# Optimization experiments

Measured on AMD Instinct MI355X. Metric: run time of the kernel, lower is better.

## Reference

```python
import jax, jax.numpy as jnp
import numpy as np

FM = 256          # feature_maps
ROUNDS = 32
N_VARS = 4000
N_CLAUSES = 16800 # ~4.2 * n_vars (3-SAT phase transition)
K = 3             # literals per clause
EPS = 1e-8


def setup_inputs() -> dict:
    key = jax.random.key(0)
    ks = jax.random.split(key, 20)

    def nrm(k, shape):
        # tf.initializers.RandomNormal default stddev = 0.05
        return jax.random.normal(k, shape, jnp.float32) * 0.05

    vs = jax.random.randint(ks[0], (N_CLAUSES, K), 1, N_VARS + 1)
    sg = jnp.where(jax.random.uniform(ks[1], (N_CLAUSES, K)) < 0.5, -1, 1)
    return {
        "clause_lits": (vs * sg).astype(jnp.int32),  # signed 1-based literals
        "n_vars": N_VARS,
        "L_init": nrm(ks[2], (1, FM)), "C_init": nrm(ks[3], (1, FM)),
        "LC_W0": nrm(ks[4], (FM, FM)), "LC_b0": jnp.zeros((FM,), jnp.float32),
        "LC_W1": nrm(ks[5], (FM, FM)), "LC_b1": jnp.zeros((FM,), jnp.float32),
        "LC_W2": nrm(ks[6], (FM, FM)), "LC_b2": jnp.zeros((FM,), jnp.float32),
        "CL_W0": nrm(ks[7], (FM, FM)), "CL_b0": jnp.zeros((FM,), jnp.float32),
        "CL_W1": nrm(ks[8], (FM, FM)), "CL_b1": jnp.zeros((FM,), jnp.float32),
        "CL_W2": nrm(ks[9], (FM, FM)), "CL_b2": jnp.zeros((FM,), jnp.float32),
        "C_Wx": nrm(ks[10], (FM, 4 * FM)), "C_Wh": nrm(ks[11], (FM, 4 * FM)),
        "C_b": jnp.zeros((4 * FM,), jnp.float32),
        "L_Wx": nrm(ks[12], (2 * FM, 4 * FM)), "L_Wh": nrm(ks[13], (FM, 4 * FM)),
        "L_b": jnp.zeros((4 * FM,), jnp.float32),
        "V_W0": nrm(ks[14], (2 * FM, 2 * FM)), "V_b0": jnp.zeros((2 * FM,), jnp.float32),
        "V_W1": nrm(ks[15], (2 * FM, 2 * FM)), "V_b1": jnp.zeros((2 * FM,), jnp.float32),
        "V_W2": nrm(ks[16], (2 * FM, 1)), "V_b2": jnp.zeros((1,), jnp.float32),
    }


def _mlp3(x, W0, b0, W1, b1, W2, b2):
    h = jax.nn.relu(x @ W0 + b0)
    h = jax.nn.relu(h @ W1 + b1)
    return h @ W2 + b2


def _lstm(x, h, c, Wx, Wh, b):
    # keras LSTMCell: gate order i, f, g, o; sigmoid recurrent, tanh activation
    z = x @ Wx + h @ Wh + b
    i, f, g, o = jnp.split(z, 4, axis=1)
    c = jax.nn.sigmoid(f) * c + jax.nn.sigmoid(i) * jnp.tanh(g)
    h = jax.nn.sigmoid(o) * jnp.tanh(c)
    return h, c


def reference(clause_lits, n_vars, L_init, C_init,
              LC_W0, LC_b0, LC_W1, LC_b1, LC_W2, LC_b2,
              CL_W0, CL_b0, CL_W1, CL_b1, CL_W2, CL_b2,
              C_Wx, C_Wh, C_b, L_Wx, L_Wh, L_b,
              V_W0, V_b0, V_W1, V_b1, V_W2, V_b2):
    n_clauses = clause_lits.shape[0]
    n_lits = 2 * n_vars
    lits = clause_lits.reshape(-1)                         # [E]
    sign = jnp.sign(lits).astype(jnp.float32)              # [E]
    var_idx = jnp.abs(lits) - 1                            # [E] 0-based var
    lit_idx = jnp.where(lits > 0, var_idx, n_vars + var_idx)
    clause_idx = jnp.repeat(jnp.arange(n_clauses), clause_lits.shape[1])

    denom = jnp.sqrt(jnp.float32(FM))
    l_h = jnp.tile(L_init / denom, (n_lits, 1))
    c_h = jnp.tile(C_init / denom, (n_clauses, 1))
    l_c = jnp.zeros_like(l_h)
    c_c = jnp.zeros_like(c_h)

    def vote(lh):
        variables = jnp.concatenate([lh[:n_vars], lh[n_vars:]], axis=1)  # [n_vars, 2*FM]
        return _mlp3(variables, V_W0, V_b0, V_W1, V_b1, V_W2, V_b2)      # [n_vars, 1]

    def clause_loss(logits):
        # softplus_log_square_loss: clause_val = exp(-sum_lit softplus(sign*logit))
        vals = logits[var_idx, 0] * sign                   # [E]
        s = jax.ops.segment_sum(jax.nn.softplus(vals), clause_idx,
                                num_segments=n_clauses, indices_are_sorted=True)
        cv = jnp.exp(-s)
        return jnp.sum(jnp.square(-jnp.log(1.0 - cv + EPS)))

    def round_fn(carry, _):
        lh, lc, ch, cc, loss = carry
        lc_pre = _mlp3(lh, LC_W0, LC_b0, LC_W1, LC_b1, LC_W2, LC_b2)
        # SpMM adj^T @ msgs: scatter literal messages into clauses
        lc_msgs = jax.ops.segment_sum(lc_pre[lit_idx], clause_idx,
                                      num_segments=n_clauses, indices_are_sorted=True)
        ch, cc = _lstm(lc_msgs, ch, cc, C_Wx, C_Wh, C_b)
        cl_pre = _mlp3(ch, CL_W0, CL_b0, CL_W1, CL_b1, CL_W2, CL_b2)
        # SpMM adj @ msgs: scatter clause messages into literals
        cl_msgs = jax.ops.segment_sum(cl_pre[clause_idx], lit_idx, num_segments=n_lits)
        flipped = jnp.concatenate([lh[n_vars:], lh[:n_vars]], axis=0)
        lh, lc = _lstm(jnp.concatenate([cl_msgs, flipped], axis=1), lh, lc,
                       L_Wx, L_Wh, L_b)
        loss = loss + clause_loss(vote(lh))
        return (lh, lc, ch, cc, loss), None

    (l_h, l_c, c_h, c_c, loss), _ = jax.lax.scan(
        round_fn, (l_h, l_c, c_h, c_c, jnp.float32(0.0)), None, length=ROUNDS)
    logits = vote(l_h)
    return logits, loss / jnp.float32(ROUNDS)
```

## Files before the change

### kernel.cpp

```cpp
#include <hip/hip_runtime.h>
#include <hip/hip_bf16.h>

#define NV 4000
#define NL 8000
#define NC 16800
#define NE 50400
#define FM 256
#define ROUNDS 32

typedef short s16x8 __attribute__((ext_vector_type(8)));
typedef __bf16 b16x8 __attribute__((ext_vector_type(8)));
typedef float f32x4 __attribute__((ext_vector_type(4)));
union V8 { s16x8 s; b16x8 b; ushort u[8]; };

using gaddr_t = const void __attribute__((address_space(1)))*;
using laddr_t = void __attribute__((address_space(3)))*;

__device__ __forceinline__ float b2f(ushort u) {
    union { uint i; float f; } v; v.i = ((uint)u) << 16; return v.f;
}
__device__ __forceinline__ ushort f2b(float f) {
    __hip_bfloat16 h = __float2bfloat16(f);
    return *(ushort*)&h;
}

__global__ void zero_kernel(float* __restrict__ p, int n) {
    int i = blockIdx.x * blockDim.x + threadIdx.x;
    if (i < n) p[i] = 0.0f;
}
__global__ void f2b_kernel(const float* __restrict__ src, ushort* __restrict__ dst, int n) {
    int i = blockIdx.x * blockDim.x + threadIdx.x;
    if (i < n) dst[i] = f2b(src[i]);
}
__global__ void transpose_w6_kernel(
    const float* __restrict__ s0, const float* __restrict__ s1, const float* __restrict__ s2,
    const float* __restrict__ s3, const float* __restrict__ s4, const float* __restrict__ s5,
    ushort* __restrict__ d0, ushort* __restrict__ d1, ushort* __restrict__ d2,
    ushort* __restrict__ d3, ushort* __restrict__ d4, ushort* __restrict__ d5)
{
    const float* srcs[6] = {s0, s1, s2, s3, s4, s5};
    ushort* dsts[6] = {d0, d1, d2, d3, d4, d5};
    const float* in = srcs[blockIdx.y];
    ushort* out = dsts[blockIdx.y];
    int idx = blockIdx.x * blockDim.x + threadIdx.x;
    int n = idx >> 8, k = idx & 255;
    out[n * 256 + k] = f2b(in[k * 256 + n]);
}
__global__ void transpose_w_kernel(const float* __restrict__ in, ushort* __restrict__ out,
                                   int K, int N, int ldo, int koff, int perm) {
    int idx = blockIdx.x * blockDim.x + threadIdx.x;
    if (idx >= K * N) return;
    int n = idx / K, k = idx - n * K;
    int row = perm ? ((n & 255) * 4 + (n >> 8)) : n;
    out[(size_t)row * ldo + koff + k] = f2b(in[(size_t)k * N + n]);
}
__global__ void permute_bias_kernel(const float* __restrict__ b, float* __restrict__ bp) {
    int n = blockIdx.x * blockDim.x + threadIdx.x;
    if (n < 1024) bp[(n & 255) * 4 + (n >> 8)] = b[n];
}

__global__ void init_all_kernel(const float* __restrict__ Li, const float* __restrict__ Ci,
                                ushort* __restrict__ lh, float* __restrict__ lc32,
                                ushort* __restrict__ ch, float* __restrict__ cc32) {
    int idx = blockIdx.x * blockDim.x + threadIdx.x;
    if (idx < NL * FM) { lh[idx] = f2b(Li[idx & 255] * (1.0f / 16.0f)); lc32[idx] = 0.0f; }
    if (idx < NC * FM) { ch[idx] = f2b(Ci[idx & 255] * (1.0f / 16.0f)); cc32[idx] = 0.0f; }
}
__global__ void fill_hist_kernel(float* __restrict__ hist, const float* __restrict__ b2,
                                 float* __restrict__ loss_arr) {
    int i = blockIdx.x * blockDim.x + threadIdx.x;
    if (i < ROUNDS * NV) hist[i] = b2[0];
    if (i < ROUNDS) loss_arr[i] = 0.0f;
}

__global__ void csr_count_kernel(const int* __restrict__ lits, int* __restrict__ deg) {
    int e = blockIdx.x * blockDim.x + threadIdx.x;
    if (e >= NE) return;
    int l = lits[e];
    int v = (l > 0 ? l : -l) - 1;
    int li = (l > 0) ? v : NV + v;
    atomicAdd(&deg[li], 1);
}
__global__ __launch_bounds__(1024) void csr_scan_kernel(const int* __restrict__ deg,
                                                        int* __restrict__ rowptr,
                                                        int* __restrict__ nxt) {
    __shared__ int ls[1024];
    int t = threadIdx.x;
    int base = t * 8;
    int local[8];
    int s = 0;
    #pragma unroll
    for (int i = 0; i < 8; ++i) {
        int idx = base + i;
        int d = (idx < NL) ? deg[idx] : 0;
        local[i] = s;
        s += d;
    }
    ls[t] = s;
    __syncthreads();
    for (int st = 1; st < 1024; st <<= 1) {
        int v = (t >= st) ? ls[t - st] : 0;
        __syncthreads();
        ls[t] += v;
        __syncthreads();
    }
    int prefix = (t == 0) ? 0 : ls[t - 1];
    #pragma unroll
    for (int i = 0; i < 8; ++i) {
        int idx = base + i;
        if (idx < NL) { int v = prefix + local[i]; rowptr[idx] = v; nxt[idx] = v; }
    }
    if (t == 1023) rowptr[NL] = ls[1023];
}
__global__ void csr_fill_kernel(const int* __restrict__ lits, int* __restrict__ nxt,
                                int* __restrict__ ecl) {
    int e = blockIdx.x * blockDim.x + threadIdx.x;
    if (e >= NE) return;
    int l = lits[e];
    int v = (l > 0 ? l : -l) - 1;
    int li = (l > 0) ? v : NV + v;
    int pos = atomicAdd(&nxt[li], 1);
    ecl[pos] = e / 3;
}

#define BKT 64

#define MLPR 32
__global__ __launch_bounds__(256) void mlp3_kernel(
    const ushort* __restrict__ A,
    const ushort* __restrict__ W0t, const float* __restrict__ b0,
    const ushort* __restrict__ W1t, const float* __restrict__ b1,
    const ushort* __restrict__ W2t, const float* __restrict__ b2,
    ushort* __restrict__ out, int M)
{
    __shared__ __align__(16) ushort As[MLPR * BKT];
    __shared__ __align__(16) ushort Wl[256 * BKT];
    __shared__ __align__(16) ushort Ab[MLPR * 264];
    const int tid = threadIdx.x;
    const int lane = tid & 63, wid = tid >> 6;
    const int rowBase = blockIdx.x * MLPR;
    const int lr = lane >> 3, ql = (lane & 7) ^ lr;
    const int cl16 = lane & 15, kg = lane >> 4;

    const ushort* Wt[3] = {W0t, W1t, W2t};
    const float*  bs[3] = {b0, b1, b2};

    #pragma unroll
    for (int layer = 0; layer < 3; ++layer) {
        f32x4 acc[2][4];
        #pragma unroll
        for (int i = 0; i < 2; ++i)
            #pragma unroll
            for (int j = 0; j < 4; ++j) acc[i][j] = (f32x4){0.f, 0.f, 0.f, 0.f};

        for (int kt = 0; kt < 4; ++kt) {
            __syncthreads();
            #pragma unroll
            for (int t = 0; t < 8; ++t) {
                int row = wid * 64 + t * 8 + lr;
                __builtin_amdgcn_global_load_lds(
                    (gaddr_t)(Wt[layer] + (size_t)row * 256 + kt * 64 + ql * 8),
                    (laddr_t)&Wl[(wid * 64 + t * 8) * BKT + lane * 8], 16, 0, 0);
            }
            if (layer == 0) {
                int row = rowBase + wid * 8 + lr;
                if (row > M - 1) row = M - 1;
                __builtin_amdgcn_global_load_lds(
                    (gaddr_t)(A + (size_t)row * 256 + kt * 64 + ql * 8),
                    (laddr_t)&As[wid * 512 + lane * 8], 16, 0, 0);
            }
            __syncthreads();
            #pragma unroll
            for (int s = 0; s < 2; ++s) {
                int kq8 = s * 4 + kg;
                V8 af[2], bf[4];
                #pragma unroll
                for (int i = 0; i < 2; ++i) {
                    int m = i * 16 + cl16;
                    if (layer == 0)
                        af[i].s = *(const s16x8*)&As[m * BKT + ((kq8 ^ (m & 7)) * 8)];
                    else
                        af[i].s = *(const s16x8*)&Ab[m * 264 + kt * 64 + kq8 * 8];
                }
                #pragma unroll
                for (int j = 0; j < 4; ++j) {
                    int n = wid * 64 + j * 16 + cl16;
                    bf[j].s = *(const s16x8*)&Wl[n * BKT + ((kq8 ^ (n & 7)) * 8)];
                }
                #pragma unroll
                for (int i = 0; i < 2; ++i)
                    #pragma unroll
                    for (int j = 0; j < 4; ++j)
                        acc[i][j] = __builtin_amdgcn_mfma_f32_16x16x32_bf16(
                            af[i].b, bf[j].b, acc[i][j], 0, 0, 0);
            }
        }
        __syncthreads();
        const int rq = (lane >> 4) * 4;
        #pragma unroll
        for (int i = 0; i < 2; ++i)
            #pragma unroll
            for (int r = 0; r < 4; ++r) {
                int row = i * 16 + rq + r;
                #pragma unroll
                for (int j = 0; j < 4; ++j) {
                    int col = wid * 64 + j * 16 + cl16;
                    float v = acc[i][j][r] + bs[layer][col];
                    if (layer < 2) {
                        Ab[row * 264 + col] = f2b(fmaxf(v, 0.0f));
                    } else {
                        int grow = rowBase + row;
                        if (grow < M) out[(size_t)grow * 256 + col] = f2b(v);
                    }
                }
            }
    }
}

__global__ __launch_bounds__(256) void gemm16_n64_kernel(
    const ushort* __restrict__ A0, int K0,
    const ushort* __restrict__ A1, int K1,
    const ushort* __restrict__ Bt, const float* __restrict__ bias,
    ushort* __restrict__ C, int M, int N, int relu)
{
    __shared__ __align__(16) ushort Al[128 * BKT];
    __shared__ __align__(16) ushort Bl[64 * BKT];
    const int Ktot = K0 + K1;
    const int tid = threadIdx.x;
    const int rowBase = blockIdx.y * 128, colBase = blockIdx.x * 64;
    const int lane = tid & 63, wid = tid >> 6;
    const int wm = (wid & 1) * 64, wn = (wid >> 1) * 32;
    const int lr = lane >> 3, ql = (lane & 7) ^ lr;

    f32x4 acc[4][2];
    #pragma unroll
    for (int i = 0; i < 4; ++i)
        #pragma unroll
        for (int j = 0; j < 2; ++j) acc[i][j] = (f32x4){0.f, 0.f, 0.f, 0.f};

    for (int k0 = 0; k0 < Ktot; k0 += BKT) {
        const ushort* As; int ks, lda;
        if (k0 < K0) { As = A0; ks = k0; lda = K0; }
        else         { As = A1; ks = k0 - K0; lda = K1; }
        __syncthreads();
        #pragma unroll
        for (int t = 0; t < 4; ++t) {
            int rloc = (wid * 4 + t) * 8 + lr;
            int ga = rowBase + rloc; if (ga > M - 1) ga = M - 1;
            __builtin_amdgcn_global_load_lds((gaddr_t)(As + (size_t)ga * lda + ks + ql * 8),
                                             (laddr_t)&Al[(wid * 4 + t) * 512], 16, 0, 0);
        }
        #pragma unroll
        for (int t = 0; t < 2; ++t) {
            int rloc = (wid * 2 + t) * 8 + lr;
            __builtin_amdgcn_global_load_lds((gaddr_t)(Bt + (size_t)(colBase + rloc) * Ktot + k0 + ql * 8),
                                             (laddr_t)&Bl[(wid * 2 + t) * 512], 16, 0, 0);
        }
        __syncthreads();
        const int cl = lane & 15, kg = lane >> 4;
        #pragma unroll
        for (int s = 0; s < 2; ++s) {
            V8 af[4], bf[2];
            #pragma unroll
            for (int i = 0; i < 4; ++i) {
                int m = wm + i * 16 + cl;
                af[i].s = *(const s16x8*)&Al[m * BKT + (((s * 4 + kg) ^ (m & 7)) * 8)];
            }
            #pragma unroll
            for (int j = 0; j < 2; ++j) {
                int n = wn + j * 16 + cl;
                bf[j].s = *(const s16x8*)&Bl[n * BKT + (((s * 4 + kg) ^ (n & 7)) * 8)];
            }
            #pragma unroll
            for (int i = 0; i < 4; ++i)
                #pragma unroll
                for (int j = 0; j < 2; ++j)
                    acc[i][j] = __builtin_amdgcn_mfma_f32_16x16x32_bf16(af[i].b, bf[j].b,
                                                                        acc[i][j], 0, 0, 0);
        }
    }
    const int rq = (lane >> 4) * 4, cl = lane & 15;
    #pragma unroll
    for (int i = 0; i < 4; ++i)
        #pragma unroll
        for (int r = 0; r < 4; ++r) {
            int grow = rowBase + wm + i * 16 + rq + r;
            if (grow >= M) continue;
            #pragma unroll
            for (int j = 0; j < 2; ++j) {
                int gcol = colBase + wn + j * 16 + cl;
                float v = acc[i][j][r] + bias[gcol];
                if (relu) v = fmaxf(v, 0.0f);
                C[(size_t)grow * N + gcol] = f2b(v);
            }
        }
}

__global__ __launch_bounds__(256) void gemm16_vote_kernel(
    const ushort* __restrict__ A0,
    const ushort* __restrict__ Bt,
    const float* __restrict__ bias,
    const ushort* __restrict__ w2,
    float* __restrict__ logits, int M)
{
    __shared__ __align__(16) ushort Al[128 * BKT];
    __shared__ __align__(16) ushort Bl[64 * BKT];
    const int Ktot = 512;
    const int tid = threadIdx.x;
    const int rowBase = blockIdx.y * 128, colBase = blockIdx.x * 64;
    const int lane = tid & 63, wid = tid >> 6;
    const int wm = (wid & 1) * 64, wn = (wid >> 1) * 32;
    const int lr = lane >> 3, ql = (lane & 7) ^ lr;

    f32x4 acc[4][2];
    #pragma unroll
    for (int i = 0; i < 4; ++i)
        #pragma unroll
        for (int j = 0; j < 2; ++j) acc[i][j] = (f32x4){0.f, 0.f, 0.f, 0.f};

    for (int k0 = 0; k0 < Ktot; k0 += BKT) {
        __syncthreads();
        #pragma unroll
        for (int t = 0; t < 4; ++t) {
            int rloc = (wid * 4 + t) * 8 + lr;
            int ga = rowBase + rloc; if (ga > M - 1) ga = M - 1;
            __builtin_amdgcn_global_load_lds((gaddr_t)(A0 + (size_t)ga * Ktot + k0 + ql * 8),
                                             (laddr_t)&Al[(wid * 4 + t) * 512], 16, 0, 0);
        }
        #pragma unroll
        for (int t = 0; t < 2; ++t) {
            int rloc = (wid * 2 + t) * 8 + lr;
            __builtin_amdgcn_global_load_lds((gaddr_t)(Bt + (size_t)(colBase + rloc) * Ktot + k0 + ql * 8),
                                             (laddr_t)&Bl[(wid * 2 + t) * 512], 16, 0, 0);
        }
        __syncthreads();
        const int cl = lane & 15, kg = lane >> 4;
        #pragma unroll
        for (int s = 0; s < 2; ++s) {
            V8 af[4], bf[2];
            #pragma unroll
            for (int i = 0; i < 4; ++i) {
                int m = wm + i * 16 + cl;
                af[i].s = *(const s16x8*)&Al[m * BKT + (((s * 4 + kg) ^ (m & 7)) * 8)];
            }
            #pragma unroll
            for (int j = 0; j < 2; ++j) {
                int n = wn + j * 16 + cl;
                bf[j].s = *(const s16x8*)&Bl[n * BKT + (((s * 4 + kg) ^ (n & 7)) * 8)];
            }
            #pragma unroll
            for (int i = 0; i < 4; ++i)
                #pragma unroll
                for (int j = 0; j < 2; ++j)
                    acc[i][j] = __builtin_amdgcn_mfma_f32_16x16x32_bf16(af[i].b, bf[j].b,
                                                                        acc[i][j], 0, 0, 0);
        }
    }
    const int rq = (lane >> 4) * 4, cl = lane & 15;
    #pragma unroll
    for (int i = 0; i < 4; ++i)
        #pragma unroll
        for (int r = 0; r < 4; ++r) {
            int grow = rowBase + wm + i * 16 + rq + r;
            float s = 0.0f;
            #pragma unroll
            for (int j = 0; j < 2; ++j) {
                int gcol = colBase + wn + j * 16 + cl;
                float h1 = b2f(f2b(fmaxf(acc[i][j][r] + bias[gcol], 0.0f)));
                s += h1 * b2f(w2[gcol]);
            }
            s += __shfl_xor(s, 1);
            s += __shfl_xor(s, 2);
            s += __shfl_xor(s, 4);
            s += __shfl_xor(s, 8);
            if (cl == 0 && grow < M) atomicAdd(&logits[grow], s);
        }
}

__global__ __launch_bounds__(256) void gemm_lstm_kernel(
    const ushort* __restrict__ A0, int K0,
    const ushort* __restrict__ A1, int K1,
    const ushort* __restrict__ A2, int K2,
    int flip1,
    const ushort* __restrict__ Bt, const float* __restrict__ biasP,
    float* __restrict__ c32, ushort* __restrict__ h_out, int M)
{
    __shared__ __align__(16) ushort smem[2 * 128 * BKT];
    ushort* Al = smem;
    ushort* Bl = smem + 128 * BKT;
    const int Ktot = K0 + K1 + K2;
    const int tid = threadIdx.x;
    const int rowBase = blockIdx.y * 128, colBase = blockIdx.x * 128;
    const int lane = tid & 63, wid = tid >> 6;
    const int wm = (wid >> 1) * 64, wn = (wid & 1) * 64;
    const int lr = lane >> 3, ql = (lane & 7) ^ lr;

    f32x4 acc[4][4];
    #pragma unroll
    for (int i = 0; i < 4; ++i)
        #pragma unroll
        for (int j = 0; j < 4; ++j) acc[i][j] = (f32x4){0.f, 0.f, 0.f, 0.f};

    for (int k0 = 0; k0 < Ktot; k0 += BKT) {
        const ushort* As; int ks, lda, flip;
        if (k0 < K0)           { As = A0; ks = k0;           lda = K0; flip = 0; }
        else if (k0 < K0 + K1) { As = A1; ks = k0 - K0;      lda = K1; flip = flip1; }
        else                   { As = A2; ks = k0 - K0 - K1; lda = K2; flip = 0; }
        __syncthreads();
        #pragma unroll
        for (int t = 0; t < 4; ++t) {
            int rloc = (wid * 4 + t) * 8 + lr;
            int ga = rowBase + rloc; if (ga > M - 1) ga = M - 1;
            if (flip) ga = (ga < NV) ? ga + NV : ga - NV;
            __builtin_amdgcn_global_load_lds((gaddr_t)(As + (size_t)ga * lda + ks + ql * 8),
                                             (laddr_t)&Al[(wid * 4 + t) * 512], 16, 0, 0);
            __builtin_amdgcn_global_load_lds((gaddr_t)(Bt + (size_t)(colBase + rloc) * Ktot + k0 + ql * 8),
                                             (laddr_t)&Bl[(wid * 4 + t) * 512], 16, 0, 0);
        }
        __syncthreads();
        const int cl = lane & 15, kg = lane >> 4;
        #pragma unroll
        for (int s = 0; s < 2; ++s) {
            V8 af[4], bf[4];
            #pragma unroll
            for (int i = 0; i < 4; ++i) {
                int m = wm + i * 16 + cl;
                af[i].s = *(const s16x8*)&Al[m * BKT + (((s * 4 + kg) ^ (m & 7)) * 8)];
            }
            #pragma unroll
            for (int j = 0; j < 4; ++j) {
                int n = wn + j * 16 + cl;
                bf[j].s = *(const s16x8*)&Bl[n * BKT + (((s * 4 + kg) ^ (n & 7)) * 8)];
            }
            #pragma unroll
            for (int i = 0; i < 4; ++i)
                #pragma unroll
                for (int j = 0; j < 4; ++j)
                    acc[i][j] = __builtin_amdgcn_mfma_f32_16x16x32_bf16(af[i].b, bf[j].b,
                                                                        acc[i][j], 0, 0, 0);
        }
    }
    __syncthreads();
    {
        const int rq = (lane >> 4) * 4, cl = lane & 15;
        #pragma unroll
        for (int i = 0; i < 4; ++i)
            #pragma unroll
            for (int r = 0; r < 4; ++r) {
                int rl = wm + i * 16 + rq + r;
                #pragma unroll
                for (int j = 0; j < 4; ++j) {
                    int clc = wn + j * 16 + cl;
                    smem[rl * 128 + clc] = f2b(acc[i][j][r] + biasP[colBase + clc]);
                }
            }
    }
    __syncthreads();
    const int fl = tid & 31, rg = tid >> 5;
    const int fglob = (colBase >> 2) + fl;
    #pragma unroll
    for (int k = 0; k < 16; ++k) {
        int rl = rg + 8 * k;
        int grow = rowBase + rl;
        if (grow >= M) continue;
        ushort4 g4 = *(const ushort4*)&smem[rl * 128 + fl * 4];
        float zi = b2f(g4.x), zf = b2f(g4.y), zg = b2f(g4.z), zo = b2f(g4.w);
        size_t ci = (size_t)grow * FM + fglob;
        float cold = c32[ci];
        float si = 1.0f / (1.0f + __expf(-zi));
        float sf = 1.0f / (1.0f + __expf(-zf));
        float so = 1.0f / (1.0f + __expf(-zo));
        float cn = sf * cold + si * tanhf(zg);
        float hn = so * tanhf(cn);
        c32[ci] = cn;
        h_out[ci] = f2b(hn);
    }
}

__global__ void gather_lc8_kernel(const ushort* __restrict__ pre, const int* __restrict__ lits,
                                  ushort* __restrict__ out) {
    int idx = blockIdx.x * blockDim.x + threadIdx.x;
    if (idx >= NC * 32) return;
    int c = idx >> 5, f8 = (idx & 31) * 8;
    const int* cl = lits + c * 3;
    float s[8] = {};
    #pragma unroll
    for (int k = 0; k < 3; ++k) {
        int l = cl[k];
        int v = (l > 0 ? l : -l) - 1;
        int li = (l > 0) ? v : NV + v;
        V8 x; x.s = *(const s16x8*)&pre[(size_t)li * FM + f8];
        #pragma unroll
        for (int e = 0; e < 8; ++e) s[e] += b2f(x.u[e]);
    }
    V8 o;
    #pragma unroll
    for (int e = 0; e < 8; ++e) o.u[e] = f2b(s[e]);
    *(s16x8*)&out[(size_t)c * FM + f8] = o.s;
}

__global__ void gather_cl8_kernel(const ushort* __restrict__ pre, const int* __restrict__ rowptr,
                                  const int* __restrict__ ecl, ushort* __restrict__ out) {
    int idx = blockIdx.x * blockDim.x + threadIdx.x;
    if (idx >= NL * 32) return;
    int li = idx >> 5, f8 = (idx & 31) * 8;
    int j0 = rowptr[li], j1 = rowptr[li + 1];
    float s[8] = {};
    for (int j = j0; j < j1; ++j) {
        V8 x; x.s = *(const s16x8*)&pre[(size_t)ecl[j] * FM + f8];
        #pragma unroll
        for (int e = 0; e < 8; ++e) s[e] += b2f(x.u[e]);
    }
    V8 o;
    #pragma unroll
    for (int e = 0; e < 8; ++e) o.u[e] = f2b(s[e]);
    *(s16x8*)&out[(size_t)li * FM + f8] = o.s;
}

__global__ __launch_bounds__(256) void loss_all_kernel(
    const float* __restrict__ logits_hist, const int* __restrict__ lits,
    float* __restrict__ loss_arr)
{
    __shared__ float sm[256];
    const int r = blockIdx.y;
    const float* logits = logits_hist + (size_t)r * NV;
    int c = blockIdx.x * 256 + threadIdx.x;
    float t2 = 0.0f;
    if (c < NC) {
        const int* cl = lits + c * 3;
        float s = 0.0f;
        #pragma unroll
        for (int k = 0; k < 3; ++k) {
            int l = cl[k];
            int v = (l > 0 ? l : -l) - 1;
            float sg = (l > 0) ? 1.0f : -1.0f;
            float val = logits[v] * sg;
            s += fmaxf(val, 0.0f) + log1pf(__expf(-fabsf(val)));
        }
        float cv = __expf(-s);
        float t = -logf(1.0f - cv + 1e-8f);
        t2 = t * t;
    }
    sm[threadIdx.x] = t2;
    __syncthreads();
    for (int st = 128; st > 0; st >>= 1) {
        if (threadIdx.x < st) sm[threadIdx.x] += sm[threadIdx.x + st];
        __syncthreads();
    }
    if (threadIdx.x == 0) atomicAdd(&loss_arr[r], sm[0]);
}

__global__ void final_out_kernel(const float* __restrict__ logits_hist,
                                 const float* __restrict__ loss_arr,
                                 float* __restrict__ out) {
    int i = blockIdx.x * blockDim.x + threadIdx.x;
    if (i < NV) out[i] = logits_hist[(size_t)(ROUNDS - 1) * NV + i];
    if (i == NV) {
        float s = 0.0f;
        for (int r = 0; r < ROUNDS; ++r) s += loss_arr[r];
        out[NV] = s * (1.0f / (float)ROUNDS);
    }
}

extern "C" void kernel_launch(void* const* d_in, const int* in_sizes, int n_in,
                              void* d_out, int out_size, void* d_ws, size_t ws_size,
                              hipStream_t stream) {
    const int* lits = (const int*)d_in[0];
    float* out = (float*)d_out;

    const float* Li   = (const float*)d_in[2];
    const float* Ci   = (const float*)d_in[3];
    const float* LCW0 = (const float*)d_in[4];
    const float* LCb0 = (const float*)d_in[5];
    const float* LCW1 = (const float*)d_in[6];
    const float* LCb1 = (const float*)d_in[7];
    const float* LCW2 = (const float*)d_in[8];
    const float* LCb2 = (const float*)d_in[9];
    const float* CLW0 = (const float*)d_in[10];
    const float* CLb0 = (const float*)d_in[11];
    const float* CLW1 = (const float*)d_in[12];
    const float* CLb1 = (const float*)d_in[13];
    const float* CLW2 = (const float*)d_in[14];
    const float* CLb2 = (const float*)d_in[15];
    const float* CWx  = (const float*)d_in[16];
    const float* CWh  = (const float*)d_in[17];
    const float* Cb   = (const float*)d_in[18];
    const float* LWx  = (const float*)d_in[19];
    const float* LWh  = (const float*)d_in[20];
    const float* Lb   = (const float*)d_in[21];
    const float* VW0  = (const float*)d_in[22];
    const float* Vb0  = (const float*)d_in[23];
    const float* VW1  = (const float*)d_in[24];
    const float* Vb1  = (const float*)d_in[25];
    const float* VW2  = (const float*)d_in[26];
    const float* Vb2  = (const float*)d_in[27];
    (void)in_sizes; (void)n_in; (void)out_size; (void)ws_size;

    char* base = (char*)d_ws;
    size_t off = 0;
    auto allocB = [&](size_t bytes) {
        void* p = base + off;
        off += (bytes + 15) & ~(size_t)15;
        return p;
    };
    float*  loss_arr    = (float*)allocB(ROUNDS * 4);
    float*  logits_hist = (float*)allocB((size_t)ROUNDS * NV * 4);
    float*  lc32        = (float*)allocB((size_t)NL * FM * 4);
    float*  cc32        = (float*)allocB((size_t)NC * FM * 4);
    float*  Cb_p        = (float*)allocB(1024 * 4);
    float*  Lb_p        = (float*)allocB(1024 * 4);
    int*    deg         = (int*)allocB(NL * 4);
    int*    rowptr      = (int*)allocB((NL + 1) * 4);
    int*    nxt         = (int*)allocB(NL * 4);
    int*    ecl         = (int*)allocB(NE * 4);
    ushort* LC0t = (ushort*)allocB((size_t)256 * 256 * 2);
    ushort* LC1t = (ushort*)allocB((size_t)256 * 256 * 2);
    ushort* LC2t = (ushort*)allocB((size_t)256 * 256 * 2);
    ushort* CL0t = (ushort*)allocB((size_t)256 * 256 * 2);
    ushort* CL1t = (ushort*)allocB((size_t)256 * 256 * 2);
    ushort* CL2t = (ushort*)allocB((size_t)256 * 256 * 2);
    ushort* CWt  = (ushort*)allocB((size_t)1024 * 512 * 2);
    ushort* LWt  = (ushort*)allocB((size_t)1024 * 768 * 2);
    ushort* VW0t = (ushort*)allocB((size_t)512 * 512 * 2);
    ushort* VW1t = (ushort*)allocB((size_t)512 * 512 * 2);
    ushort* vw2  = (ushort*)allocB((size_t)512 * 2);
    ushort* lh_a = (ushort*)allocB((size_t)NL * FM * 2);
    ushort* lh_b = (ushort*)allocB((size_t)NL * FM * 2);
    ushort* ch_a = (ushort*)allocB((size_t)NC * FM * 2);
    ushort* ch_b = (ushort*)allocB((size_t)NC * FM * 2);
    ushort* lcm16 = (ushort*)allocB((size_t)NC * FM * 2);
    ushort* clm16 = (ushort*)allocB((size_t)NL * FM * 2);
    ushort* tL    = (ushort*)allocB((size_t)NL * FM * 2);
    ushort* tC    = (ushort*)allocB((size_t)NC * FM * 2);
    ushort* v0    = (ushort*)allocB((size_t)NV * 512 * 2);

    hipLaunchKernelGGL(transpose_w6_kernel, dim3(256, 6), dim3(256), 0, stream,
                       LCW0, LCW1, LCW2, CLW0, CLW1, CLW2,
                       LC0t, LC1t, LC2t, CL0t, CL1t, CL2t);
    auto tw = [&](const float* in, ushort* o, int K, int N, int ldo, int koff, int perm) {
        hipLaunchKernelGGL(transpose_w_kernel, dim3((K * N + 255) / 256), dim3(256), 0, stream,
                           in, o, K, N, ldo, koff, perm);
    };
    tw(CWx,  CWt, 256, 1024, 512, 0, 1);
    tw(CWh,  CWt, 256, 1024, 512, 256, 1);
    tw(LWx,  LWt, 512, 1024, 768, 0, 1);
    tw(LWh,  LWt, 256, 1024, 768, 512, 1);
    tw(VW0,  VW0t, 512, 512, 512, 0, 0);
    tw(VW1,  VW1t, 512, 512, 512, 0, 0);
    hipLaunchKernelGGL(f2b_kernel, dim3(2), dim3(256), 0, stream, VW2, vw2, 512);
    hipLaunchKernelGGL(permute_bias_kernel, dim3(4), dim3(256), 0, stream, Cb, Cb_p);
    hipLaunchKernelGGL(permute_bias_kernel, dim3(4), dim3(256), 0, stream, Lb, Lb_p);
    hipLaunchKernelGGL(init_all_kernel, dim3(NC * FM / 256), dim3(256), 0, stream,
                       Li, Ci, lh_a, lc32, ch_a, cc32);
    hipLaunchKernelGGL(fill_hist_kernel, dim3((ROUNDS * NV + 255) / 256), dim3(256), 0, stream,
                       logits_hist, Vb2, loss_arr);
    hipLaunchKernelGGL(zero_kernel, dim3((NL + 255) / 256), dim3(256), 0, stream, (float*)deg, NL);
    hipLaunchKernelGGL(csr_count_kernel, dim3((NE + 255) / 256), dim3(256), 0, stream, lits, deg);
    hipLaunchKernelGGL(csr_scan_kernel, dim3(1), dim3(1024), 0, stream, deg, rowptr, nxt);
    hipLaunchKernelGGL(csr_fill_kernel, dim3((NE + 255) / 256), dim3(256), 0, stream, lits, nxt, ecl);

    ushort *lh_c = lh_a, *lh_n = lh_b, *ch_c = ch_a, *ch_n = ch_b;

    for (int r = 0; r < ROUNDS; ++r) {
        hipLaunchKernelGGL(mlp3_kernel, dim3(NL / MLPR), dim3(256), 0, stream,
                           lh_c, LC0t, LCb0, LC1t, LCb1, LC2t, LCb2, tL, NL);
        hipLaunchKernelGGL(gather_lc8_kernel, dim3(NC * 32 / 256), dim3(256), 0, stream,
                           tL, lits, lcm16);
        hipLaunchKernelGGL(gemm_lstm_kernel, dim3(8, (NC + 127) / 128), dim3(256), 0, stream,
                           lcm16, 256, ch_c, 256, (const ushort*)0, 0, 0,
                           CWt, Cb_p, cc32, ch_n, NC);
        hipLaunchKernelGGL(mlp3_kernel, dim3(NC / MLPR, 1), dim3(256), 0, stream,
                           ch_n, CL0t, CLb0, CL1t, CLb1, CL2t, CLb2, tC, NC);
        hipLaunchKernelGGL(gather_cl8_kernel, dim3(NL * 32 / 256), dim3(256), 0, stream,
                           tC, rowptr, ecl, clm16);
        hipLaunchKernelGGL(gemm_lstm_kernel, dim3(8, (NL + 127) / 128), dim3(256), 0, stream,
                           clm16, 256, lh_c, 256, lh_c, 256, 1,
                           LWt, Lb_p, lc32, lh_n, NL);
        hipLaunchKernelGGL(gemm16_n64_kernel, dim3(8, (NV + 127) / 128), dim3(256), 0, stream,
                           lh_n, 256, lh_n + (size_t)NV * FM, 256, VW0t, Vb0, v0, NV, 512, 1);
        hipLaunchKernelGGL(gemm16_vote_kernel, dim3(8, (NV + 127) / 128), dim3(256), 0, stream,
                           v0, VW1t, Vb1, vw2, logits_hist + (size_t)r * NV, NV);
        ushort* tswap;
        tswap = lh_c; lh_c = lh_n; lh_n = tswap;
        tswap = ch_c; ch_c = ch_n; ch_n = tswap;
    }

    hipLaunchKernelGGL(loss_all_kernel, dim3((NC + 255) / 256, ROUNDS), dim3(256), 0, stream,
                       logits_hist, lits, loss_arr);
    hipLaunchKernelGGL(final_out_kernel, dim3((NV + 256) / 256), dim3(256), 0, stream,
                       logits_hist, loss_arr, out);
}
```

Before: 5.397 ms.

## Double-buffer LDS tiles in MLP and GEMM kernels to overlap loads with MFMA

Doubles the LDS staging buffers in the fused 3-layer MLP kernel, the generic bf16 GEMM kernel and the vote GEMM kernel. The next K-tile is issued with async global-to-LDS loads while the current tile feeds the MFMAs, so each k-step needs one barrier instead of two. The MLP kernel is flattened into a single 12-step pipeline across its three layers, with an extra barrier before layer 1 writes its activations back to shared memory. This raises per-block LDS use, which may lower occupancy. Overlap also depends on the compiler not inserting a full vmcnt wait before the LDS reads.

```diff
diff --git a/kernel.cpp b/kernel.cpp
--- a/kernel.cpp
+++ b/kernel.cpp
@@ -133,8 +133,8 @@
     const ushort* __restrict__ W2t, const float* __restrict__ b2,
     ushort* __restrict__ out, int M)
 {
-    __shared__ __align__(16) ushort As[MLPR * BKT];
-    __shared__ __align__(16) ushort Wl[256 * BKT];
+    __shared__ __align__(16) ushort As[2][MLPR * BKT];
+    __shared__ __align__(16) ushort Wl[2][256 * BKT];
     __shared__ __align__(16) ushort Ab[MLPR * 264];
     const int tid = threadIdx.x;
     const int lane = tid & 63, wid = tid >> 6;
@@ -145,75 +145,84 @@
     const ushort* Wt[3] = {W0t, W1t, W2t};
     const float*  bs[3] = {b0, b1, b2};
 
-    #pragma unroll
-    for (int layer = 0; layer < 3; ++layer) {
-        f32x4 acc[2][4];
-        #pragma unroll
-        for (int i = 0; i < 2; ++i)
-            #pragma unroll
-            for (int j = 0; j < 4; ++j) acc[i][j] = (f32x4){0.f, 0.f, 0.f, 0.f};
-
-        for (int kt = 0; kt < 4; ++kt) {
-            __syncthreads();
-            #pragma unroll
-            for (int t = 0; t < 8; ++t) {
-                int row = wid * 64 + t * 8 + lr;
-                __builtin_amdgcn_global_load_lds(
-                    (gaddr_t)(Wt[layer] + (size_t)row * 256 + kt * 64 + ql * 8),
-                    (laddr_t)&Wl[(wid * 64 + t * 8) * BKT + lane * 8], 16, 0, 0);
-            }
-            if (layer == 0) {
-                int row = rowBase + wid * 8 + lr;
-                if (row > M - 1) row = M - 1;
-                __builtin_amdgcn_global_load_lds(
-                    (gaddr_t)(A + (size_t)row * 256 + kt * 64 + ql * 8),
-                    (laddr_t)&As[wid * 512 + lane * 8], 16, 0, 0);
-            }
-            __syncthreads();
-            #pragma unroll
-            for (int s = 0; s < 2; ++s) {
-                int kq8 = s * 4 + kg;
-                V8 af[2], bf[4];
+    auto stage = [&](int t, int p) {
+        int layer = t >> 2, kt = t & 3;
+        #pragma unroll
+        for (int q = 0; q < 8; ++q) {
+            int row = wid * 64 + q * 8 + lr;
+            __builtin_amdgcn_global_load_lds(
+                (gaddr_t)(Wt[layer] + (size_t)row * 256 + kt * 64 + ql * 8),
+                (laddr_t)&Wl[p][(wid * 64 + q * 8) * BKT + lane * 8], 16, 0, 0);
+        }
+        if (t < 4) {
+            int row = rowBase + wid * 8 + lr;
+            if (row > M - 1) row = M - 1;
+            __builtin_amdgcn_global_load_lds(
+                (gaddr_t)(A + (size_t)row * 256 + kt * 64 + ql * 8),
+                (laddr_t)&As[p][wid * 512 + lane * 8], 16, 0, 0);
+        }
+    };
+
+    f32x4 acc[2][4];
+    #pragma unroll
+    for (int i = 0; i < 2; ++i)
+        #pragma unroll
+        for (int j = 0; j < 4; ++j) acc[i][j] = (f32x4){0.f, 0.f, 0.f, 0.f};
+
+    stage(0, 0);
+    for (int t = 0; t < 12; ++t) {
+        const int layer = t >> 2, kt = t & 3, p = t & 1;
+        __syncthreads();
+        if (t + 1 < 12) stage(t + 1, (t + 1) & 1);
+        #pragma unroll
+        for (int s = 0; s < 2; ++s) {
+            int kq8 = s * 4 + kg;
+            V8 af[2], bf[4];
+            #pragma unroll
+            for (int i = 0; i < 2; ++i) {
+                int m = i * 16 + cl16;
+                if (layer == 0)
+                    af[i].s = *(const s16x8*)&As[p][m * BKT + ((kq8 ^ (m & 7)) * 8)];
+                else
+                    af[i].s = *(const s16x8*)&Ab[m * 264 + kt * 64 + kq8 * 8];
+            }
+            #pragma unroll
+            for (int j = 0; j < 4; ++j) {
+                int n = wid * 64 + j * 16 + cl16;
+                bf[j].s = *(const s16x8*)&Wl[p][n * BKT + ((kq8 ^ (n & 7)) * 8)];
+            }
+            #pragma unroll
+            for (int i = 0; i < 2; ++i)
                 #pragma unroll
-                for (int i = 0; i < 2; ++i) {
-                    int m = i * 16 + cl16;
-                    if (layer == 0)
-                        af[i].s = *(const s16x8*)&As[m * BKT + ((kq8 ^ (m & 7)) * 8)];
-                    else
-                        af[i].s = *(const s16x8*)&Ab[m * 264 + kt * 64 + kq8 * 8];
-                }
+                for (int j = 0; j < 4; ++j)
+                    acc[i][j] = __builtin_amdgcn_mfma_f32_16x16x32_bf16(
+                        af[i].b, bf[j].b, acc[i][j], 0, 0, 0);
+        }
+        if (kt == 3) {
+            if (layer == 1) __syncthreads();
+            const int rq = (lane >> 4) * 4;
+            #pragma unroll
+            for (int i = 0; i < 2; ++i)
                 #pragma unroll
-                for (int j = 0; j < 4; ++j) {
-                    int n = wid * 64 + j * 16 + cl16;
-                    bf[j].s = *(const s16x8*)&Wl[n * BKT + ((kq8 ^ (n & 7)) * 8)];
-                }
-                #pragma unroll
-                for (int i = 0; i < 2; ++i)
+                for (int r = 0; r < 4; ++r) {
+                    int row = i * 16 + rq + r;
                     #pragma unroll
-                    for (int j = 0; j < 4; ++j)
-                        acc[i][j] = __builtin_amdgcn_mfma_f32_16x16x32_bf16(
-                            af[i].b, bf[j].b, acc[i][j], 0, 0, 0);
-            }
-        }
-        __syncthreads();
-        const int rq = (lane >> 4) * 4;
-        #pragma unroll
-        for (int i = 0; i < 2; ++i)
-            #pragma unroll
-            for (int r = 0; r < 4; ++r) {
-                int row = i * 16 + rq + r;
-                #pragma unroll
-                for (int j = 0; j < 4; ++j) {
-                    int col = wid * 64 + j * 16 + cl16;
-                    float v = acc[i][j][r] + bs[layer][col];
-                    if (layer < 2) {
-                        Ab[row * 264 + col] = f2b(fmaxf(v, 0.0f));
-                    } else {
-                        int grow = rowBase + row;
-                        if (grow < M) out[(size_t)grow * 256 + col] = f2b(v);
+                    for (int j = 0; j < 4; ++j) {
+                        int col = wid * 64 + j * 16 + cl16;
+                        float v = acc[i][j][r] + bs[layer][col];
+                        if (layer < 2) {
+                            Ab[row * 264 + col] = f2b(fmaxf(v, 0.0f));
+                        } else {
+                            int grow = rowBase + row;
+                            if (grow < M) out[(size_t)grow * 256 + col] = f2b(v);
+                        }
                     }
                 }
-            }
+            #pragma unroll
+            for (int i = 0; i < 2; ++i)
+                #pragma unroll
+                for (int j = 0; j < 4; ++j) acc[i][j] = (f32x4){0.f, 0.f, 0.f, 0.f};
+        }
     }
 }
 
@@ -223,40 +232,47 @@
     const ushort* __restrict__ Bt, const float* __restrict__ bias,
     ushort* __restrict__ C, int M, int N, int relu)
 {
-    __shared__ __align__(16) ushort Al[128 * BKT];
-    __shared__ __align__(16) ushort Bl[64 * BKT];
+    __shared__ __align__(16) ushort Al[2][128 * BKT];
+    __shared__ __align__(16) ushort Bl[2][64 * BKT];
     const int Ktot = K0 + K1;
+    const int nk = Ktot / BKT;
     const int tid = threadIdx.x;
     const int rowBase = blockIdx.y * 128, colBase = blockIdx.x * 64;
     const int lane = tid & 63, wid = tid >> 6;
     const int wm = (wid & 1) * 64, wn = (wid >> 1) * 32;
     const int lr = lane >> 3, ql = (lane & 7) ^ lr;
 
-    f32x4 acc[4][2];
-    #pragma unroll
-    for (int i = 0; i < 4; ++i)
-        #pragma unroll
-        for (int j = 0; j < 2; ++j) acc[i][j] = (f32x4){0.f, 0.f, 0.f, 0.f};
-
-    for (int k0 = 0; k0 < Ktot; k0 += BKT) {
+    auto stage = [&](int kc, int p) {
+        int k0 = kc * BKT;
         const ushort* As; int ks, lda;
         if (k0 < K0) { As = A0; ks = k0; lda = K0; }
         else         { As = A1; ks = k0 - K0; lda = K1; }
-        __syncthreads();
         #pragma unroll
         for (int t = 0; t < 4; ++t) {
             int rloc = (wid * 4 + t) * 8 + lr;
             int ga = rowBase + rloc; if (ga > M - 1) ga = M - 1;
             __builtin_amdgcn_global_load_lds((gaddr_t)(As + (size_t)ga * lda + ks + ql * 8),
-                                             (laddr_t)&Al[(wid * 4 + t) * 512], 16, 0, 0);
+                                             (laddr_t)&Al[p][(wid * 4 + t) * 512], 16, 0, 0);
         }
         #pragma unroll
         for (int t = 0; t < 2; ++t) {
             int rloc = (wid * 2 + t) * 8 + lr;
             __builtin_amdgcn_global_load_lds((gaddr_t)(Bt + (size_t)(colBase + rloc) * Ktot + k0 + ql * 8),
-                                             (laddr_t)&Bl[(wid * 2 + t) * 512], 16, 0, 0);
-        }
+                                             (laddr_t)&Bl[p][(wid * 2 + t) * 512], 16, 0, 0);
+        }
+    };
+
+    f32x4 acc[4][2];
+    #pragma unroll
+    for (int i = 0; i < 4; ++i)
+        #pragma unroll
+        for (int j = 0; j < 2; ++j) acc[i][j] = (f32x4){0.f, 0.f, 0.f, 0.f};
+
+    stage(0, 0);
+    for (int kc = 0; kc < nk; ++kc) {
         __syncthreads();
+        if (kc + 1 < nk) stage(kc + 1, (kc + 1) & 1);
+        const int p = kc & 1;
         const int cl = lane & 15, kg = lane >> 4;
         #pragma unroll
         for (int s = 0; s < 2; ++s) {
@@ -264,12 +280,12 @@
             #pragma unroll
             for (int i = 0; i < 4; ++i) {
                 int m = wm + i * 16 + cl;
-                af[i].s = *(const s16x8*)&Al[m * BKT + (((s * 4 + kg) ^ (m & 7)) * 8)];
+                af[i].s = *(const s16x8*)&Al[p][m * BKT + (((s * 4 + kg) ^ (m & 7)) * 8)];
             }
             #pragma unroll
             for (int j = 0; j < 2; ++j) {
                 int n = wn + j * 16 + cl;
-                bf[j].s = *(const s16x8*)&Bl[n * BKT + (((s * 4 + kg) ^ (n & 7)) * 8)];
+                bf[j].s = *(const s16x8*)&Bl[p][n * BKT + (((s * 4 + kg) ^ (n & 7)) * 8)];
             }
             #pragma unroll
             for (int i = 0; i < 4; ++i)
@@ -303,37 +319,44 @@
     const ushort* __restrict__ w2,
     float* __restrict__ logits, int M)
 {
-    __shared__ __align__(16) ushort Al[128 * BKT];
-    __shared__ __align__(16) ushort Bl[64 * BKT];
+    __shared__ __align__(16) ushort Al[2][128 * BKT];
+    __shared__ __align__(16) ushort Bl[2][64 * BKT];
     const int Ktot = 512;
+    const int nk = Ktot / BKT;
     const int tid = threadIdx.x;
     const int rowBase = blockIdx.y * 128, colBase = blockIdx.x * 64;
     const int lane = tid & 63, wid = tid >> 6;
     const int wm = (wid & 1) * 64, wn = (wid >> 1) * 32;
     const int lr = lane >> 3, ql = (lane & 7) ^ lr;
 
-    f32x4 acc[4][2];
-    #pragma unroll
-    for (int i = 0; i < 4; ++i)
-        #pragma unroll
-        for (int j = 0; j < 2; ++j) acc[i][j] = (f32x4){0.f, 0.f, 0.f, 0.f};
-
-    for (int k0 = 0; k0 < Ktot; k0 += BKT) {
-        __syncthreads();
+    auto stage = [&](int kc, int p) {
+        int k0 = kc * BKT;
         #pragma unroll
         for (int t = 0; t < 4; ++t) {
             int rloc = (wid * 4 + t) * 8 + lr;
             int ga = rowBase + rloc; if (ga > M - 1) ga = M - 1;
             __builtin_amdgcn_global_load_lds((gaddr_t)(A0 + (size_t)ga * Ktot + k0 + ql * 8),
-                                             (laddr_t)&Al[(wid * 4 + t) * 512], 16, 0, 0);
+                                             (laddr_t)&Al[p][(wid * 4 + t) * 512], 16, 0, 0);
         }
         #pragma unroll
         for (int t = 0; t < 2; ++t) {
             int rloc = (wid * 2 + t) * 8 + lr;
             __builtin_amdgcn_global_load_lds((gaddr_t)(Bt + (size_t)(colBase + rloc) * Ktot + k0 + ql * 8),
-                                             (laddr_t)&Bl[(wid * 2 + t) * 512], 16, 0, 0);
-        }
+                                             (laddr_t)&Bl[p][(wid * 2 + t) * 512], 16, 0, 0);
+        }
+    };
+
+    f32x4 acc[4][2];
+    #pragma unroll
+    for (int i = 0; i < 4; ++i)
+        #pragma unroll
+        for (int j = 0; j < 2; ++j) acc[i][j] = (f32x4){0.f, 0.f, 0.f, 0.f};
+
+    stage(0, 0);
+    for (int kc = 0; kc < nk; ++kc) {
         __syncthreads();
+        if (kc + 1 < nk) stage(kc + 1, (kc + 1) & 1);
+        const int p = kc & 1;
         const int cl = lane & 15, kg = lane >> 4;
         #pragma unroll
         for (int s = 0; s < 2; ++s) {
@@ -341,12 +364,12 @@
             #pragma unroll
             for (int i = 0; i < 4; ++i) {
                 int m = wm + i * 16 + cl;
-                af[i].s = *(const s16x8*)&Al[m * BKT + (((s * 4 + kg) ^ (m & 7)) * 8)];
+                af[i].s = *(const s16x8*)&Al[p][m * BKT + (((s * 4 + kg) ^ (m & 7)) * 8)];
             }
             #pragma unroll
             for (int j = 0; j < 2; ++j) {
                 int n = wn + j * 16 + cl;
-                bf[j].s = *(const s16x8*)&Bl[n * BKT + (((s * 4 + kg) ^ (n & 7)) * 8)];
+                bf[j].s = *(const s16x8*)&Bl[p][n * BKT + (((s * 4 + kg) ^ (n & 7)) * 8)];
             }
             #pragma unroll
             for (int i = 0; i < 4; ++i)
```

Result: slower. 5.801 ms (+7.5%).

## Fuse literal-to-clause gather into clause LSTM GEMM A-tile load

Applied to the files above, without the earlier changes.

Removes the separate gather_lc8 kernel and its intermediate lcm16 buffer. The clause LSTM GEMM now sums the three literal message rows directly into its LDS A tile while loading the first K block. This saves one launch per round and a write plus re-read of an NC x 256 bf16 buffer. In exchange, the gather is repeated by each of the 8 column blocks, and the A load becomes synchronous vector loads instead of async global_load_lds.

```diff
diff --git a/kernel.cpp b/kernel.cpp
--- a/kernel.cpp
+++ b/kernel.cpp
@@ -381,7 +381,7 @@
     const ushort* __restrict__ A0, int K0,
     const ushort* __restrict__ A1, int K1,
     const ushort* __restrict__ A2, int K2,
-    int flip1,
+    int flip1, const int* __restrict__ glits,
     const ushort* __restrict__ Bt, const float* __restrict__ biasP,
     float* __restrict__ c32, ushort* __restrict__ h_out, int M)
 {
@@ -407,13 +407,40 @@
         else if (k0 < K0 + K1) { As = A1; ks = k0 - K0;      lda = K1; flip = flip1; }
         else                   { As = A2; ks = k0 - K0 - K1; lda = K2; flip = 0; }
         __syncthreads();
+        if (glits && k0 < K0) {
+            #pragma unroll
+            for (int t = 0; t < 4; ++t) {
+                int rloc = (wid * 4 + t) * 8 + lr;
+                int c = rowBase + rloc; if (c > M - 1) c = M - 1;
+                const int* cl3 = glits + c * 3;
+                float s[8] = {};
+                #pragma unroll
+                for (int kk = 0; kk < 3; ++kk) {
+                    int l = cl3[kk];
+                    int v = (l > 0 ? l : -l) - 1;
+                    int li = (l > 0) ? v : NV + v;
+                    V8 x; x.s = *(const s16x8*)&A0[(size_t)li * 256 + ks + ql * 8];
+                    #pragma unroll
+                    for (int e = 0; e < 8; ++e) s[e] += b2f(x.u[e]);
+                }
+                V8 o;
+                #pragma unroll
+                for (int e = 0; e < 8; ++e) o.u[e] = f2b(s[e]);
+                *(s16x8*)&Al[(wid * 4 + t) * 512 + lane * 8] = o.s;
+            }
+        } else {
+            #pragma unroll
+            for (int t = 0; t < 4; ++t) {
+                int rloc = (wid * 4 + t) * 8 + lr;
+                int ga = rowBase + rloc; if (ga > M - 1) ga = M - 1;
+                if (flip) ga = (ga < NV) ? ga + NV : ga - NV;
+                __builtin_amdgcn_global_load_lds((gaddr_t)(As + (size_t)ga * lda + ks + ql * 8),
+                                                 (laddr_t)&Al[(wid * 4 + t) * 512], 16, 0, 0);
+            }
+        }
         #pragma unroll
         for (int t = 0; t < 4; ++t) {
             int rloc = (wid * 4 + t) * 8 + lr;
-            int ga = rowBase + rloc; if (ga > M - 1) ga = M - 1;
-            if (flip) ga = (ga < NV) ? ga + NV : ga - NV;
-            __builtin_amdgcn_global_load_lds((gaddr_t)(As + (size_t)ga * lda + ks + ql * 8),
-                                             (laddr_t)&Al[(wid * 4 + t) * 512], 16, 0, 0);
             __builtin_amdgcn_global_load_lds((gaddr_t)(Bt + (size_t)(colBase + rloc) * Ktot + k0 + ql * 8),
                                              (laddr_t)&Bl[(wid * 4 + t) * 512], 16, 0, 0);
         }
@@ -475,28 +502,6 @@
         c32[ci] = cn;
         h_out[ci] = f2b(hn);
     }
-}
-
-__global__ void gather_lc8_kernel(const ushort* __restrict__ pre, const int* __restrict__ lits,
-                                  ushort* __restrict__ out) {
-    int idx = blockIdx.x * blockDim.x + threadIdx.x;
-    if (idx >= NC * 32) return;
-    int c = idx >> 5, f8 = (idx & 31) * 8;
-    const int* cl = lits + c * 3;
-    float s[8] = {};
-    #pragma unroll
-    for (int k = 0; k < 3; ++k) {
-        int l = cl[k];
-        int v = (l > 0 ? l : -l) - 1;
-        int li = (l > 0) ? v : NV + v;
-        V8 x; x.s = *(const s16x8*)&pre[(size_t)li * FM + f8];
-        #pragma unroll
-        for (int e = 0; e < 8; ++e) s[e] += b2f(x.u[e]);
-    }
-    V8 o;
-    #pragma unroll
-    for (int e = 0; e < 8; ++e) o.u[e] = f2b(s[e]);
-    *(s16x8*)&out[(size_t)c * FM + f8] = o.s;
 }
 
 __global__ void gather_cl8_kernel(const ushort* __restrict__ pre, const int* __restrict__ rowptr,
@@ -628,7 +633,6 @@
     ushort* lh_b = (ushort*)allocB((size_t)NL * FM * 2);
     ushort* ch_a = (ushort*)allocB((size_t)NC * FM * 2);
     ushort* ch_b = (ushort*)allocB((size_t)NC * FM * 2);
-    ushort* lcm16 = (ushort*)allocB((size_t)NC * FM * 2);
     ushort* clm16 = (ushort*)allocB((size_t)NL * FM * 2);
     ushort* tL    = (ushort*)allocB((size_t)NL * FM * 2);
     ushort* tC    = (ushort*)allocB((size_t)NC * FM * 2);
@@ -664,17 +668,15 @@
     for (int r = 0; r < ROUNDS; ++r) {
         hipLaunchKernelGGL(mlp3_kernel, dim3(NL / MLPR), dim3(256), 0, stream,
                            lh_c, LC0t, LCb0, LC1t, LCb1, LC2t, LCb2, tL, NL);
-        hipLaunchKernelGGL(gather_lc8_kernel, dim3(NC * 32 / 256), dim3(256), 0, stream,
-                           tL, lits, lcm16);
         hipLaunchKernelGGL(gemm_lstm_kernel, dim3(8, (NC + 127) / 128), dim3(256), 0, stream,
-                           lcm16, 256, ch_c, 256, (const ushort*)0, 0, 0,
+                           tL, 256, ch_c, 256, (const ushort*)0, 0, 0, lits,
                            CWt, Cb_p, cc32, ch_n, NC);
         hipLaunchKernelGGL(mlp3_kernel, dim3(NC / MLPR, 1), dim3(256), 0, stream,
                            ch_n, CL0t, CLb0, CL1t, CLb1, CL2t, CLb2, tC, NC);
         hipLaunchKernelGGL(gather_cl8_kernel, dim3(NL * 32 / 256), dim3(256), 0, stream,
                            tC, rowptr, ecl, clm16);
         hipLaunchKernelGGL(gemm_lstm_kernel, dim3(8, (NL + 127) / 128), dim3(256), 0, stream,
-                           clm16, 256, lh_c, 256, lh_c, 256, 1,
+                           clm16, 256, lh_c, 256, lh_c, 256, 1, (const int*)0,
                            LWt, Lb_p, lc32, lh_n, NL);
         hipLaunchKernelGGL(gemm16_n64_kernel, dim3(8, (NV + 127) / 128), dim3(256), 0, stream,
                            lh_n, 256, lh_n + (size_t)NV * FM, 256, VW0t, Vb0, v0, NV, 512, 1);
```

After: 6.017 ms. 1.11x slower.
